# Optimization experiments

Hardware: AMD Instinct MI355X
Metric: run time of the kernel (lower is better)

Reference implementation:

```python
import jax, jax.numpy as jnp
import numpy as np
import math

B, N, OBS, H, A = 4096, 64, 64, 64, 8


def setup_inputs() -> dict:
    key = jax.random.key(0)
    kit = iter(jax.random.split(key, 64))

    def W(o, i):
        return jax.random.normal(next(kit), (o, i), jnp.float32) / float(np.sqrt(i))

    def bvec(o):
        return jax.random.normal(next(kit), (o,), jnp.float32) * 0.01

    inp = {
        "x": jax.random.normal(next(kit), (B, N, OBS), jnp.float32),
        "rnd_nums": jax.random.uniform(next(kit), (B, N), dtype=jnp.float32),
        "idx": jax.random.randint(next(kit), (B, N), 0, N),
    }
    inp.update(embed_w=W(H, OBS), embed_b=bvec(H))
    for pre in ("ia", "c1", "c2"):  # init_attn, consensus_attn1, consensus_attn2 (1 head)
        inp.update({pre + "_wq": W(H, H), pre + "_bq": bvec(H),
                    pre + "_wk": W(H, H), pre + "_bk": bvec(H),
                    pre + "_wv": W(H, H), pre + "_bv": bvec(H),
                    pre + "_wo": W(H, H), pre + "_bo": bvec(H)})
    inp.update(msg_w=W(H, H), msg_b=bvec(H), st_w=W(H, H), st_b=bvec(H),
               mean_w=W(A, 2 * H), mean_b=bvec(A), ls_w=W(A, 2 * H), ls_b=bvec(A))
    return inp


def reference(x, rnd_nums, idx, embed_w, embed_b,
              ia_wq, ia_bq, ia_wk, ia_bk, ia_wv, ia_bv, ia_wo, ia_bo,
              msg_w, msg_b, st_w, st_b,
              c1_wq, c1_bq, c1_wk, c1_bk, c1_wv, c1_bv, c1_wo, c1_bo,
              c2_wq, c2_bq, c2_wk, c2_bk, c2_wv, c2_bv, c2_wo, c2_bo,
              mean_w, mean_b, ls_w, ls_b):
    h = embed_w.shape[0]
    scale = 1.0 / math.sqrt(h)
    lrelu = lambda z: jax.nn.leaky_relu(z, 0.2)

    # ---- initial state estimation (self-attention over agents) ----
    e = lrelu(x @ embed_w.T + embed_b)                       # [B,N,H]
    q = e @ ia_wq.T + ia_bq
    k = e @ ia_wk.T + ia_bk
    v = e @ ia_wv.T + ia_bv
    w = jax.nn.softmax(jnp.einsum('bih,bjh->bij', q, k) * scale, axis=-1)
    attn = jnp.tanh(jnp.einsum('bij,bjh->bih', w, v) @ ia_wo.T + ia_bo)
    messages = attn @ msg_w.T + msg_b                        # [B,N,H]
    temp = attn @ st_w.T + st_b                              # [B,N,H]

    # ---- consensus masks: mg[b,i,j] = (r_i > a_i) | (r_j > a_i) ----
    a = jnp.take_along_axis(rnd_nums, idx, axis=1)           # agent_rnd per agent slot [B,N]
    gi = rnd_nums[:, :, None] > a[:, :, None]
    gj = rnd_nums[:, None, :] > a[:, :, None]
    mg = (gi | gj).astype(x.dtype)                           # [B,N,N]
    ml = 1.0 - mg

    def cons(mask, wq, bq, wk, bk, wv, bv, wo, bo):
        # single-token query (agent temp state) attends over zero-masked messages;
        # masked tokens contribute k = bk, v = bv (bias survives the zeroing).
        qq = temp @ wq.T + bq                                # [B,N,H]
        km = messages @ wk.T                                 # [B,N,H] (no bias; folded below)
        vm = messages @ wv.T
        s = (mask * jnp.einsum('bih,bjh->bij', qq, km) + (qq @ bk)[:, :, None]) * scale
        wgt = jax.nn.softmax(s, axis=-1)                     # [B,N_agents,N_tokens]
        ctx = jnp.einsum('bij,bjh->bih', wgt * mask, vm) + bv
        return ctx @ wo.T + bo

    o1 = cons(mg, c1_wq, c1_bq, c1_wk, c1_bk, c1_wv, c1_bv, c1_wo, c1_bo)
    o2 = cons(ml, c2_wq, c2_bq, c2_wk, c2_bk, c2_wv, c2_bv, c2_wo, c2_bo)
    out = lrelu(jnp.concatenate([o1, o2], axis=-1))          # [B,N,2H]
    mean = out @ mean_w.T + mean_b                           # [B,N,A]
    logstd = jnp.clip(out @ ls_w.T + ls_b, -20.0, 2.0)
    return mean, jnp.exp(logstd)
```

## Files before the change

### kernel.cpp

```cpp
#include <hip/hip_runtime.h>

namespace {

typedef __bf16 bf16x8 __attribute__((ext_vector_type(8)));
typedef float f32x4 __attribute__((ext_vector_type(4)));
typedef unsigned int uint4v __attribute__((ext_vector_type(4)));

#define MFMA16(a,b,c) __builtin_amdgcn_mfma_f32_16x16x32_bf16((a),(b),(c),0,0,0)

constexpr float SCALE = 0.125f;

constexpr int WS_HW  = 57344;
constexpr int WS_NV  = 61440;
constexpr int WS_VEC = 63488;
constexpr int WS_SC  = 65536;

__device__ __forceinline__ int PI(int c){ return 4*(c&15) + (c>>4); }
__device__ __forceinline__ int PINV(int p){ return 16*(p&3) + (p>>2); }

__device__ __forceinline__ unsigned short f2b(float f){
  return __builtin_bit_cast(unsigned short, (__bf16)f);
}
__device__ __forceinline__ unsigned pack2(float a, float b){
  return (unsigned)f2b(a) | ((unsigned)f2b(b)<<16);
}
template<int ACT>
__device__ __forceinline__ float actf(float v){
  if constexpr (ACT==1) return v>0.f ? v : 0.2f*v;
  else if constexpr (ACT==2) return 1.f - 2.f/(__expf(2.f*v)+1.f);
  else return v;
}

struct PrepP {
  const float *embed_w, *mean_w, *ls_w;
  const float *ia_wq, *ia_bq, *ia_wk, *ia_wv, *ia_wo, *ia_bv, *ia_bo;
  const float *c1_wq, *c1_bq, *c1_wk, *c1_bk, *c1_wv, *c1_bv, *c1_wo, *c1_bo;
  const float *c2_wq, *c2_bq, *c2_wk, *c2_bk, *c2_wv, *c2_bv, *c2_wo, *c2_bo;
  const float *msg_w, *msg_b, *st_w, *st_b;
  char* ws;
};

__device__ void mmAB_f32(const float* A, const float* B, float* O){
  const int t=threadIdx.x, r=t>>2, c0=(t&3)*16;
  float acc[16];
  #pragma unroll
  for(int j=0;j<16;j++) acc[j]=0.f;
  for(int h=0;h<64;h++){
    const float a=A[r*64+h];
    #pragma unroll
    for(int j=0;j<16;j++) acc[j]=fmaf(a,B[h*64+c0+j],acc[j]);
  }
  #pragma unroll
  for(int j=0;j<16;j++) O[r*64+c0+j]=acc[j];
}
__device__ void mmAB_bf(const float* A, const float* B, __bf16* D){
  const int t=threadIdx.x, r=t>>2, c0=(t&3)*16;
  float acc[16];
  #pragma unroll
  for(int j=0;j<16;j++) acc[j]=0.f;
  for(int h=0;h<64;h++){
    const float a=A[r*64+h];
    #pragma unroll
    for(int j=0;j<16;j++) acc[j]=fmaf(a,B[h*64+c0+j],acc[j]);
  }
  #pragma unroll
  for(int j=0;j<16;j++) D[r*64+PI(c0+j)]=(__bf16)acc[j];
}
__device__ void mmTA_bfx(const float* A, const float* B, __bf16* D){
  const int t=threadIdx.x, a=t>>2, b0=(t&3)*16;
  float acc[16];
  #pragma unroll
  for(int j=0;j<16;j++) acc[j]=0.f;
  for(int h=0;h<64;h++){
    const float av=A[h*64+a];
    #pragma unroll
    for(int j=0;j<16;j++) acc[j]=fmaf(av,B[h*64+b0+j],acc[j]);
  }
  #pragma unroll
  for(int j=0;j<16;j++) D[a*64 + (PI(b0+j) ^ ((a&7)<<3))]=(__bf16)acc[j];
}

__global__ void prep_kernel(PrepP q){
  __shared__ float PF[2][4096];
  __shared__ float hv[64], gv[64];
  const int job=blockIdx.x, t=threadIdx.x;
  char* ws=q.ws;
  float* VECF=(float*)(ws+WS_VEC);
  float* SCF =(float*)(ws+WS_SC);
  __bf16* NVD=(__bf16*)(ws+WS_NV);

  if(job==0){
    __bf16* emb=(__bf16*)(ws+0*8192);
    #pragma unroll
    for(int i=0;i<16;i++){
      const int idx=t*16+i, o=idx>>6, pp=idx&63;
      emb[idx]=(__bf16)q.embed_w[o*64 + PINV(pp ^ ((o&7)<<3))];
    }
    __bf16* hw=(__bf16*)(ws+WS_HW);
    #pragma unroll
    for(int i=0;i<8;i++){
      const int flat=t*8+i, o=flat>>7, qq=flat&127, half=qq>>6, pp=qq&63;
      const float v=(o<8)?q.mean_w[o*128+half*64+PINV(pp)]
                         :q.ls_w[(o-8)*128+half*64+PINV(pp)];
      hw[flat]=(__bf16)v;
    }
    #pragma unroll
    for(int i=0;i<3;i++){ const int id=t*3+i; if(id<768) NVD[256+id]=(__bf16)0.f; }
  } else if(job==1){
    mmTA_bfx(q.ia_wk, q.ia_wq, (__bf16*)(ws+1*8192));
    if(t<64){ float s=0; for(int h=0;h<64;h++) s+=q.ia_wk[h*64+t]*q.ia_bq[h]; VECF[t]=s; }
  } else if(job==2){
    mmAB_bf(q.ia_wo, q.ia_wv, (__bf16*)(ws+2*8192));
    if(t<64){ float s=q.ia_bo[t]; for(int h=0;h<64;h++) s+=q.ia_wo[t*64+h]*q.ia_bv[h];
              VECF[64+t]=s; }
  } else if(job==3 || job==5){
    const int cons=(job==3)?0:1;
    const float *wq=cons?q.c2_wq:q.c1_wq, *bq=cons?q.c2_bq:q.c1_bq;
    const float *wk=cons?q.c2_wk:q.c1_wk, *bk=cons?q.c2_bk:q.c1_bk;
    mmAB_f32(wq, q.st_w, PF[0]);
    if(t<64){ float s=bq[t]; for(int k=0;k<64;k++) s+=wq[t*64+k]*q.st_b[k]; hv[t]=s; }
    __syncthreads();
    mmAB_f32(wk, q.msg_w, PF[1]);
    if(t<64){ float s=0; for(int k=0;k<64;k++) s+=wk[t*64+k]*q.msg_b[k]; gv[t]=s; }
    __syncthreads();
    mmTA_bfx(PF[1], PF[0], (__bf16*)(ws+(cons?5:3)*8192));
    if(t<64){
      float s=0; for(int h=0;h<64;h++) s+=PF[1][h*64+t]*hv[h];
      VECF[128+cons*64+t]=s;
      float s0=0,s1=0;
      for(int h=0;h<64;h++){ s0+=PF[0][h*64+t]*gv[h]; s1+=PF[0][h*64+t]*bk[h]; }
      NVD[(2*cons  )*64+PI(t)]=(__bf16)s0;
      NVD[(2*cons+1)*64+PI(t)]=(__bf16)s1;
    }
    if(t==0){
      float c=0,hb=0;
      for(int i=0;i<64;i++){ c+=hv[i]*gv[i]; hb+=hv[i]*bk[i]; }
      SCF[2*cons]=c; SCF[2*cons+1]=hb;
    }
  } else {
    const int cons=(job==4)?0:1;
    const float *wo=cons?q.c2_wo:q.c1_wo, *wvv=cons?q.c2_wv:q.c1_wv;
    const float *bv=cons?q.c2_bv:q.c1_bv, *bo=cons?q.c2_bo:q.c1_bo;
    mmAB_f32(wo, wvv, PF[0]);
    if(t<64){ float s=bo[t]; for(int h=0;h<64;h++) s+=wo[t*64+h]*bv[h];
              VECF[320+cons*128+t]=s; }
    __syncthreads();
    mmAB_bf(PF[0], q.msg_w, (__bf16*)(ws+(cons?6:4)*8192));
    if(t<64){ float s=0; for(int k=0;k<64;k++) s+=PF[0][t*64+k]*q.msg_b[k];
              VECF[256+cons*128+t]=s; }
  }
}

struct Params {
  const float *x, *rnd; const int *idx;
  const float *embed_b, *mean_b, *ls_b;
  const char* ws; float* out; int std_off;
};

__device__ __forceinline__ bf16x8 fragld(const char* buf, int row, int kb){
  const int byte = row*128 + (kb ^ ((row&7)<<4));
  return __builtin_bit_cast(bf16x8, *reinterpret_cast<const uint4v*>(buf + byte));
}
__device__ __forceinline__ bf16x8 gld(const char* a){
  return __builtin_bit_cast(bf16x8, *reinterpret_cast<const uint4v*>(a));
}
__device__ __forceinline__ void stageT(const char* src, char* L, int t){
  __builtin_amdgcn_global_load_lds(
      (const __attribute__((address_space(1))) unsigned int*)(src + t*16),
      (__attribute__((address_space(3))) unsigned int*)(L + (t>>6)*1024), 16, 0, 0);
}
__device__ __forceinline__ void loadB_lds(const char* Bl, bf16x8* bf, int fr, int fg){
  #pragma unroll
  for(int n=0;n<4;n++){
    bf[2*n]   = fragld(Bl, n*16+fr, fg*16);
    bf[2*n+1] = fragld(Bl, n*16+fr, 64+fg*16);
  }
}

__device__ __forceinline__ void mm_AB(const char* A, const char* Bl, f32x4* acc,
                                      int fr,int fg,int wv4){
  const bf16x8 a0=fragld(A,16*wv4+fr,fg*16), a1=fragld(A,16*wv4+fr,64+fg*16);
  #pragma unroll
  for(int n=0;n<4;n++){
    acc[n]=MFMA16(a0, fragld(Bl,n*16+fr,fg*16),    acc[n]);
    acc[n]=MFMA16(a1, fragld(Bl,n*16+fr,64+fg*16), acc[n]);
  }
}
__device__ __forceinline__ void mm_rAB(bf16x8 a0, bf16x8 a1, const bf16x8* bf,
                                       f32x4* acc){
  #pragma unroll
  for(int n=0;n<4;n++){
    acc[n]=MFMA16(a0, bf[2*n],   acc[n]);
    acc[n]=MFMA16(a1, bf[2*n+1], acc[n]);
  }
}

template<int ACT>
__device__ __forceinline__ void store_cb(char* C, const f32x4* acc, const float* bz,
                                         int fr,int fg,int wv4){
  #pragma unroll
  for(int r=0;r<4;r++){
    const int R=16*wv4+4*fg+r;
    float v[4];
    #pragma unroll
    for(int n=0;n<4;n++) v[n]=actf<ACT>(acc[n][r]+bz[n]);
    uint2 pk; pk.x=pack2(v[0],v[1]); pk.y=pack2(v[2],v[3]);
    *reinterpret_cast<uint2*>(C + R*128 + ((8*fr)^((R&7)<<4))) = pk;
  }
}
__device__ __forceinline__ void store_rb(char* C, const f32x4* acc, const float* dR,
                                         int fr,int fg,int wv4){
  #pragma unroll
  for(int r=0;r<4;r++){
    const int R=16*wv4+4*fg+r;
    float v[4];
    #pragma unroll
    for(int n=0;n<4;n++) v[n]=acc[n][r]+dR[r];
    uint2 pk; pk.x=pack2(v[0],v[1]); pk.y=pack2(v[2],v[3]);
    *reinterpret_cast<uint2*>(C + R*128 + ((8*fr)^((R&7)<<4))) = pk;
  }
}

template<int MODE>
__device__ __forceinline__ void ssoft(const char* Aq, const bf16x8* bf, char* P,
                                      const float* rs, const float* as_,
                                      const float* zu, const float* zq,
                                      float cu, float cq,
                                      int fr,int fg,int wv4){
  f32x4 acc[4];
  #pragma unroll
  for(int n=0;n<4;n++) acc[n]=f32x4{0.f,0.f,0.f,0.f};
  const bf16x8 a0=fragld(Aq,16*wv4+fr,fg*16), a1=fragld(Aq,16*wv4+fr,64+fg*16);
  #pragma unroll
  for(int n=0;n<4;n++){
    acc[n]=MFMA16(a0, bf[2*n],   acc[n]);
    acc[n]=MFMA16(a1, bf[2*n+1], acc[n]);
  }
  unsigned mbits=0;
  if constexpr(MODE!=0){
    float rc[4], aR[4], ucR[4], qtR[4]; bool giR[4];
    #pragma unroll
    for(int n=0;n<4;n++) rc[n]=rs[n*16+fr];
    #pragma unroll
    for(int r=0;r<4;r++){
      const int R=16*wv4+4*fg+r;
      aR[r]=as_[R]; giR[r]=rs[R]>aR[r];
      ucR[r]=zu[R]+cu; qtR[r]=zq[R]+cq;
    }
    #pragma unroll
    for(int n=0;n<4;n++){
      #pragma unroll
      for(int r=0;r<4;r++){
        bool mv=giR[r]||(rc[n]>aR[r]);
        if constexpr(MODE==2) mv=!mv;
        const float mf=mv?1.f:0.f;
        if(mv) mbits|=1u<<(n*4+r);
        acc[n][r]=(mf*(acc[n][r]+ucR[r])+qtR[r])*SCALE;
      }
    }
  }
  float sm[4]={0,0,0,0};
  #pragma unroll
  for(int n=0;n<4;n++){
    #pragma unroll
    for(int r=0;r<4;r++){
      float e;
      if constexpr(MODE==0) e=__expf(acc[n][r]*SCALE);
      else e=__expf(acc[n][r]);
      acc[n][r]=e; sm[r]+=e;
    }
  }
  #pragma unroll
  for(int m=1;m<16;m<<=1){
    #pragma unroll
    for(int r=0;r<4;r++) sm[r]+=__shfl_xor(sm[r],m);
  }
  #pragma unroll
  for(int r=0;r<4;r++){
    const int R=16*wv4+4*fg+r;
    const float ri=1.f/sm[r];
    float v[4];
    #pragma unroll
    for(int n=0;n<4;n++){
      float e=acc[n][r]*ri;
      if constexpr(MODE!=0) e=(mbits&(1u<<(n*4+r)))?e:0.f;
      v[n]=e;
    }
    uint2 pk; pk.x=pack2(v[0],v[1]); pk.y=pack2(v[2],v[3]);
    *reinterpret_cast<uint2*>(P + R*128 + ((8*fr)^((R&7)<<4))) = pk;
  }
}

__global__ __launch_bounds__(512,4) void rap_kernel(Params p, int Bb){
  __shared__ __align__(16) char Bact[2][3][8192];
  __shared__ __align__(16) char WSst[2][8192];
  __shared__ float rnd_s[2][64], a_s[2][64], zbuf[2][4][64];
  const int t=threadIdx.x;
  const int fr=t&15, fg=(t>>4)&3, wv=t>>6, l=t&63;
  const int item=wv>>2, wv4=wv&3;
  const int b0=blockIdx.x*2;
  const int bi=(b0+item<Bb)?(b0+item):(Bb-1);
  const char* ws=p.ws;
  const float* VECF=(const float*)(ws+WS_VEC);
  const float* SCF =(const float*)(ws+WS_SC);
  char* A0=Bact[item][0]; char* A1=Bact[item][1]; char* A2=Bact[item][2];
  char* WO1=WSst[item];
  bf16x8 bfv[8];

  stageT(ws+0*8192, WSst[0], t);
  stageT(ws+1*8192, WSst[1], t);
  if(t<128){
    const int it2=t>>6, i2=t&63;
    const int bb=(b0+it2<Bb)?(b0+it2):(Bb-1);
    rnd_s[it2][i2]=p.rnd[bb*64+i2];
    a_s[it2][i2]  =p.rnd[bb*64+p.idx[bb*64+i2]];
  }
  {
    const float* Gx=p.x+(size_t)bi*4096;
    #pragma unroll
    for(int j=0;j<2;j++){
      const int lf=j*64+l, R=16*wv4+(lf>>3), k=lf&7;
      const float2 L0=*reinterpret_cast<const float2*>(Gx+R*64+2*k);
      const float2 L1=*reinterpret_cast<const float2*>(Gx+R*64+16+2*k);
      const float2 L2=*reinterpret_cast<const float2*>(Gx+R*64+32+2*k);
      const float2 L3=*reinterpret_cast<const float2*>(Gx+R*64+48+2*k);
      uint4 pk;
      pk.x=pack2(L0.x,L1.x); pk.y=pack2(L2.x,L3.x);
      pk.z=pack2(L0.y,L1.y); pk.w=pack2(L2.y,L3.y);
      *reinterpret_cast<uint4*>(A0 + R*128 + ((16*k)^((R&7)<<4)))=pk;
    }
  }
  __syncthreads();
  { f32x4 acc[4]={{0,0,0,0},{0,0,0,0},{0,0,0,0},{0,0,0,0}};
    mm_AB(A0, WSst[0], acc, fr,fg,wv4);
    float bz[4];
    #pragma unroll
    for(int n=0;n<4;n++) bz[n]=p.embed_b[n*16+fr];
    store_cb<1>(A1, acc, bz, fr,fg,wv4); }
  { f32x4 acc[4]={{0,0,0,0},{0,0,0,0},{0,0,0,0},{0,0,0,0}};
    mm_AB(A1, WSst[1], acc, fr,fg,wv4);
    float bz[4];
    #pragma unroll
    for(int n=0;n<4;n++) bz[n]=VECF[n*16+fr];
    store_cb<0>(A0, acc, bz, fr,fg,wv4); }
  __syncthreads();
  stageT(ws+3*8192, WSst[0], t);
  stageT(ws+5*8192, WSst[1], t);
  const bf16x8 aVo0=gld(ws+2*8192+(16*wv4+fr)*128+fg*16);
  const bf16x8 aVo1=gld(ws+2*8192+(16*wv4+fr)*128+64+fg*16);
  loadB_lds(A1, bfv, fr, fg);
  ssoft<0>(A0, bfv, A0, nullptr,nullptr,nullptr,nullptr,0.f,0.f, fr,fg,wv4);
  { f32x4 acc[4]={{0,0,0,0},{0,0,0,0},{0,0,0,0},{0,0,0,0}};
    mm_rAB(aVo0, aVo1, bfv, acc);
    const float bz[4]={0,0,0,0};
    store_cb<0>(A2, acc, bz, fr,fg,wv4); }
  __syncthreads();
  const bf16x8 nv0=gld(ws+WS_NV+fr*128+fg*16);
  const bf16x8 nv1=gld(ws+WS_NV+fr*128+64+fg*16);
  { f32x4 acc[4]={{0,0,0,0},{0,0,0,0},{0,0,0,0},{0,0,0,0}};
    mm_AB(A0, A2, acc, fr,fg,wv4);
    float bz[4];
    #pragma unroll
    for(int n=0;n<4;n++) bz[n]=VECF[64+n*16+fr];
    store_cb<2>(A1, acc, bz, fr,fg,wv4); }
  { const bf16x8 a0=fragld(A1,16*wv4+fr,fg*16), a1=fragld(A1,16*wv4+fr,64+fg*16);
    f32x4 acc[4]={{0,0,0,0},{0,0,0,0},{0,0,0,0},{0,0,0,0}};
    #pragma unroll
    for(int n=0;n<4;n++){
      acc[n]=MFMA16(a0, fragld(WSst[0],n*16+fr,fg*16),    acc[n]);
      acc[n]=MFMA16(a1, fragld(WSst[0],n*16+fr,64+fg*16), acc[n]);
    }
    f32x4 za={0,0,0,0};
    za=MFMA16(a0, nv0, za);
    za=MFMA16(a1, nv1, za);
    if(fr<4){
      #pragma unroll
      for(int r=0;r<4;r++) zbuf[item][fr][16*wv4+4*fg+r]=za[r];
    }
    float bz[4];
    #pragma unroll
    for(int n=0;n<4;n++) bz[n]=VECF[128+n*16+fr];
    store_cb<0>(A0, acc, bz, fr,fg,wv4); }
  __syncthreads();
  const bf16x8 aN10=gld(ws+4*8192+(16*wv4+fr)*128+fg*16);
  const bf16x8 aN11=gld(ws+4*8192+(16*wv4+fr)*128+64+fg*16);
  loadB_lds(A1, bfv, fr, fg);
  ssoft<1>(A0, bfv, A0, rnd_s[item], a_s[item], zbuf[item][0], zbuf[item][1],
           SCF[0], SCF[1], fr,fg,wv4);
  { f32x4 acc[4]={{0,0,0,0},{0,0,0,0},{0,0,0,0},{0,0,0,0}};
    mm_rAB(aN10, aN11, bfv, acc);
    float dR[4];
    #pragma unroll
    for(int r=0;r<4;r++) dR[r]=VECF[256+16*wv4+4*fg+r];
    store_rb(A2, acc, dR, fr,fg,wv4); }
  __syncthreads();
  f32x4 o1acc[4]={{0,0,0,0},{0,0,0,0},{0,0,0,0},{0,0,0,0}};
  mm_AB(A0, A2, o1acc, fr,fg,wv4);
  { f32x4 acc[4]={{0,0,0,0},{0,0,0,0},{0,0,0,0},{0,0,0,0}};
    const bf16x8 a0=fragld(A1,16*wv4+fr,fg*16), a1=fragld(A1,16*wv4+fr,64+fg*16);
    #pragma unroll
    for(int n=0;n<4;n++){
      acc[n]=MFMA16(a0, fragld(WSst[1],n*16+fr,fg*16),    acc[n]);
      acc[n]=MFMA16(a1, fragld(WSst[1],n*16+fr,64+fg*16), acc[n]);
    }
    float bz[4];
    #pragma unroll
    for(int n=0;n<4;n++) bz[n]=VECF[192+n*16+fr];
    store_cb<0>(A0, acc, bz, fr,fg,wv4); }
  __syncthreads();
  { float bz[4];
    #pragma unroll
    for(int n=0;n<4;n++) bz[n]=VECF[320+n*16+fr];
    store_cb<1>(WO1, o1acc, bz, fr,fg,wv4); }
  const bf16x8 aN20=gld(ws+6*8192+(16*wv4+fr)*128+fg*16);
  const bf16x8 aN21=gld(ws+6*8192+(16*wv4+fr)*128+64+fg*16);
  loadB_lds(A1, bfv, fr, fg);
  ssoft<2>(A0, bfv, A0, rnd_s[item], a_s[item], zbuf[item][2], zbuf[item][3],
           SCF[2], SCF[3], fr,fg,wv4);
  { f32x4 acc[4]={{0,0,0,0},{0,0,0,0},{0,0,0,0},{0,0,0,0}};
    mm_rAB(aN20, aN21, bfv, acc);
    float dR[4];
    #pragma unroll
    for(int r=0;r<4;r++) dR[r]=VECF[384+16*wv4+4*fg+r];
    store_rb(A2, acc, dR, fr,fg,wv4); }
  __syncthreads();
  bf16x8 hw[4];
  #pragma unroll
  for(int kt=0;kt<4;kt++) hw[kt]=gld(ws+WS_HW + fr*256 + kt*64 + fg*16);
  { f32x4 acc[4]={{0,0,0,0},{0,0,0,0},{0,0,0,0},{0,0,0,0}};
    mm_AB(A0, A2, acc, fr,fg,wv4);
    float bz[4];
    #pragma unroll
    for(int n=0;n<4;n++) bz[n]=VECF[448+n*16+fr];
    store_cb<1>(A1, acc, bz, fr,fg,wv4); }
  { f32x4 acc={0,0,0,0};
    #pragma unroll
    for(int kt=0;kt<4;kt++){
      const bf16x8 af=fragld(kt<2?WO1:A1, 16*wv4+fr, (kt&1)*64+fg*16);
      acc=MFMA16(af, hw[kt], acc);
    }
    if(b0+item<Bb){
      const float bz=(fr<8)?p.mean_b[fr]:p.ls_b[fr-8];
      #pragma unroll
      for(int r=0;r<4;r++){
        const int R=16*wv4+4*fg+r;
        const int g=((b0+item)*64+R)*8;
        float v=acc[r]+bz;
        if(fr<8) p.out[g+fr]=v;
        else{ v=fminf(fmaxf(v,-20.f),2.f); p.out[p.std_off+g+(fr-8)]=__expf(v); }
      }
    }
  }
}

}

extern "C" void kernel_launch(void* const* d_in, const int* in_sizes, int n_in,
                              void* d_out, int out_size, void* d_ws, size_t ws_size,
                              hipStream_t stream){
  (void)n_in; (void)out_size; (void)ws_size;
  PrepP q;
  q.embed_w=(const float*)d_in[3];
  q.ia_wq=(const float*)d_in[5];  q.ia_bq=(const float*)d_in[6];
  q.ia_wk=(const float*)d_in[7];
  q.ia_wv=(const float*)d_in[9];  q.ia_bv=(const float*)d_in[10];
  q.ia_wo=(const float*)d_in[11]; q.ia_bo=(const float*)d_in[12];
  q.c1_wq=(const float*)d_in[13]; q.c1_bq=(const float*)d_in[14];
  q.c1_wk=(const float*)d_in[15]; q.c1_bk=(const float*)d_in[16];
  q.c1_wv=(const float*)d_in[17]; q.c1_bv=(const float*)d_in[18];
  q.c1_wo=(const float*)d_in[19]; q.c1_bo=(const float*)d_in[20];
  q.c2_wq=(const float*)d_in[21]; q.c2_bq=(const float*)d_in[22];
  q.c2_wk=(const float*)d_in[23]; q.c2_bk=(const float*)d_in[24];
  q.c2_wv=(const float*)d_in[25]; q.c2_bv=(const float*)d_in[26];
  q.c2_wo=(const float*)d_in[27]; q.c2_bo=(const float*)d_in[28];
  q.msg_w=(const float*)d_in[29]; q.msg_b=(const float*)d_in[30];
  q.st_w =(const float*)d_in[31]; q.st_b =(const float*)d_in[32];
  q.mean_w=(const float*)d_in[33]; q.ls_w=(const float*)d_in[35];
  q.ws=(char*)d_ws;
  prep_kernel<<<dim3(7), dim3(256), 0, stream>>>(q);

  Params p;
  p.x  =(const float*)d_in[0];
  p.rnd=(const float*)d_in[1];
  p.idx=(const int*)  d_in[2];
  p.embed_b=(const float*)d_in[4];
  p.mean_b =(const float*)d_in[34];
  p.ls_b   =(const float*)d_in[36];
  p.ws=(const char*)d_ws;
  p.out=(float*)d_out;
  const int Bb=in_sizes[0]/4096;
  p.std_off=Bb*64*8;
  const int nb=(Bb+1)/2;
  rap_kernel<<<dim3(nb), dim3(512), 0, stream>>>(p, Bb);
}
```

Baseline: 115.8 us.

## Relax block barriers to LDS-only waits and interleave score/value matmuls

Replaces __syncthreads with inline-asm barriers. Most of them wait only on lgkmcnt, so outstanding global loads into registers can stay in flight across the barrier. Each attention stage is split into the score MFMA and a softmax post-pass, and the value/message matmul and its store now run between them to overlap MFMA work with the softmax math. It also drops a redundant reload of the shared B fragments from LDS in the second consensus stage, since that LDS tile has not changed. The risk is correctness if any barrier actually depended on pending global memory operations, and register pressure rises because the score accumulators stay live longer.

Result: slower. 121.7 us (+5.1%).

```diff
diff --git a/kernel.cpp b/kernel.cpp
--- a/kernel.cpp
+++ b/kernel.cpp
@@ -29,6 +29,13 @@
   if constexpr (ACT==1) return v>0.f ? v : 0.2f*v;
   else if constexpr (ACT==2) return 1.f - 2.f/(__expf(2.f*v)+1.f);
   else return v;
+}
+
+__device__ __forceinline__ void bar_lgkm(){
+  asm volatile("s_waitcnt lgkmcnt(0)\n\ts_barrier" ::: "memory");
+}
+__device__ __forceinline__ void bar_full(){
+  asm volatile("s_waitcnt vmcnt(0) lgkmcnt(0)\n\ts_barrier" ::: "memory");
 }
 
 struct PrepP {
@@ -186,14 +193,23 @@
     acc[n]=MFMA16(a1, fragld(Bl,n*16+fr,64+fg*16), acc[n]);
   }
 }
-__device__ __forceinline__ void mm_rAB(bf16x8 a0, bf16x8 a1, const bf16x8* bf,
-                                       f32x4* acc){
+__device__ __forceinline__ void mm_ABr(const char* A, const bf16x8* bf, f32x4* acc,
+                                       int fr,int fg,int wv4){
+  const bf16x8 a0=fragld(A,16*wv4+fr,fg*16), a1=fragld(A,16*wv4+fr,64+fg*16);
   #pragma unroll
   for(int n=0;n<4;n++){
     acc[n]=MFMA16(a0, bf[2*n],   acc[n]);
     acc[n]=MFMA16(a1, bf[2*n+1], acc[n]);
   }
 }
+__device__ __forceinline__ void mm_rAB(bf16x8 a0, bf16x8 a1, const bf16x8* bf,
+                                       f32x4* acc){
+  #pragma unroll
+  for(int n=0;n<4;n++){
+    acc[n]=MFMA16(a0, bf[2*n],   acc[n]);
+    acc[n]=MFMA16(a1, bf[2*n+1], acc[n]);
+  }
+}
 
 template<int ACT>
 __device__ __forceinline__ void store_cb(char* C, const f32x4* acc, const float* bz,
@@ -221,21 +237,21 @@
   }
 }
 
-template<int MODE>
-__device__ __forceinline__ void ssoft(const char* Aq, const bf16x8* bf, char* P,
-                                      const float* rs, const float* as_,
-                                      const float* zu, const float* zq,
-                                      float cu, float cq,
-                                      int fr,int fg,int wv4){
-  f32x4 acc[4];
-  #pragma unroll
-  for(int n=0;n<4;n++) acc[n]=f32x4{0.f,0.f,0.f,0.f};
+__device__ __forceinline__ void score_mm(const char* Aq, const bf16x8* bf, f32x4* acc,
+                                         int fr,int fg,int wv4){
   const bf16x8 a0=fragld(Aq,16*wv4+fr,fg*16), a1=fragld(Aq,16*wv4+fr,64+fg*16);
   #pragma unroll
   for(int n=0;n<4;n++){
     acc[n]=MFMA16(a0, bf[2*n],   acc[n]);
     acc[n]=MFMA16(a1, bf[2*n+1], acc[n]);
   }
+}
+template<int MODE>
+__device__ __forceinline__ void soft_post(f32x4* acc, char* P,
+                                          const float* rs, const float* as_,
+                                          const float* zu, const float* zq,
+                                          float cu, float cq,
+                                          int fr,int fg,int wv4){
   unsigned mbits=0;
   if constexpr(MODE!=0){
     float rc[4], aR[4], ucR[4], qtR[4]; bool giR[4];
@@ -330,7 +346,7 @@
       *reinterpret_cast<uint4*>(A0 + R*128 + ((16*k)^((R&7)<<4)))=pk;
     }
   }
-  __syncthreads();
+  bar_full();
   { f32x4 acc[4]={{0,0,0,0},{0,0,0,0},{0,0,0,0},{0,0,0,0}};
     mm_AB(A0, WSst[0], acc, fr,fg,wv4);
     float bz[4];
@@ -343,18 +359,20 @@
     #pragma unroll
     for(int n=0;n<4;n++) bz[n]=VECF[n*16+fr];
     store_cb<0>(A0, acc, bz, fr,fg,wv4); }
-  __syncthreads();
+  bar_lgkm();
   stageT(ws+3*8192, WSst[0], t);
   stageT(ws+5*8192, WSst[1], t);
   const bf16x8 aVo0=gld(ws+2*8192+(16*wv4+fr)*128+fg*16);
   const bf16x8 aVo1=gld(ws+2*8192+(16*wv4+fr)*128+64+fg*16);
   loadB_lds(A1, bfv, fr, fg);
-  ssoft<0>(A0, bfv, A0, nullptr,nullptr,nullptr,nullptr,0.f,0.f, fr,fg,wv4);
-  { f32x4 acc[4]={{0,0,0,0},{0,0,0,0},{0,0,0,0},{0,0,0,0}};
-    mm_rAB(aVo0, aVo1, bfv, acc);
-    const float bz[4]={0,0,0,0};
-    store_cb<0>(A2, acc, bz, fr,fg,wv4); }
-  __syncthreads();
+  { f32x4 sacc[4]={{0,0,0,0},{0,0,0,0},{0,0,0,0},{0,0,0,0}};
+    score_mm(A0, bfv, sacc, fr,fg,wv4);
+    { f32x4 acc[4]={{0,0,0,0},{0,0,0,0},{0,0,0,0},{0,0,0,0}};
+      mm_rAB(aVo0, aVo1, bfv, acc);
+      const float bz[4]={0,0,0,0};
+      store_cb<0>(A2, acc, bz, fr,fg,wv4); }
+    soft_post<0>(sacc, A0, nullptr,nullptr,nullptr,nullptr,0.f,0.f, fr,fg,wv4); }
+  bar_full();
   const bf16x8 nv0=gld(ws+WS_NV+fr*128+fg*16);
   const bf16x8 nv1=gld(ws+WS_NV+fr*128+64+fg*16);
   { f32x4 acc[4]={{0,0,0,0},{0,0,0,0},{0,0,0,0},{0,0,0,0}};
@@ -381,19 +399,21 @@
     #pragma unroll
     for(int n=0;n<4;n++) bz[n]=VECF[128+n*16+fr];
     store_cb<0>(A0, acc, bz, fr,fg,wv4); }
-  __syncthreads();
+  bar_lgkm();
   const bf16x8 aN10=gld(ws+4*8192+(16*wv4+fr)*128+fg*16);
   const bf16x8 aN11=gld(ws+4*8192+(16*wv4+fr)*128+64+fg*16);
   loadB_lds(A1, bfv, fr, fg);
-  ssoft<1>(A0, bfv, A0, rnd_s[item], a_s[item], zbuf[item][0], zbuf[item][1],
-           SCF[0], SCF[1], fr,fg,wv4);
-  { f32x4 acc[4]={{0,0,0,0},{0,0,0,0},{0,0,0,0},{0,0,0,0}};
-    mm_rAB(aN10, aN11, bfv, acc);
-    float dR[4];
-    #pragma unroll
-    for(int r=0;r<4;r++) dR[r]=VECF[256+16*wv4+4*fg+r];
-    store_rb(A2, acc, dR, fr,fg,wv4); }
-  __syncthreads();
+  { f32x4 sacc[4]={{0,0,0,0},{0,0,0,0},{0,0,0,0},{0,0,0,0}};
+    score_mm(A0, bfv, sacc, fr,fg,wv4);
+    { f32x4 acc[4]={{0,0,0,0},{0,0,0,0},{0,0,0,0},{0,0,0,0}};
+      mm_rAB(aN10, aN11, bfv, acc);
+      float dR[4];
+      #pragma unroll
+      for(int r=0;r<4;r++) dR[r]=VECF[256+16*wv4+4*fg+r];
+      store_rb(A2, acc, dR, fr,fg,wv4); }
+    soft_post<1>(sacc, A0, rnd_s[item], a_s[item], zbuf[item][0], zbuf[item][1],
+                 SCF[0], SCF[1], fr,fg,wv4); }
+  bar_lgkm();
   f32x4 o1acc[4]={{0,0,0,0},{0,0,0,0},{0,0,0,0},{0,0,0,0}};
   mm_AB(A0, A2, o1acc, fr,fg,wv4);
   { f32x4 acc[4]={{0,0,0,0},{0,0,0,0},{0,0,0,0},{0,0,0,0}};
@@ -407,23 +427,24 @@
     #pragma unroll
     for(int n=0;n<4;n++) bz[n]=VECF[192+n*16+fr];
     store_cb<0>(A0, acc, bz, fr,fg,wv4); }
-  __syncthreads();
+  bar_lgkm();
   { float bz[4];
     #pragma unroll
     for(int n=0;n<4;n++) bz[n]=VECF[320+n*16+fr];
     store_cb<1>(WO1, o1acc, bz, fr,fg,wv4); }
   const bf16x8 aN20=gld(ws+6*8192+(16*wv4+fr)*128+fg*16);
   const bf16x8 aN21=gld(ws+6*8192+(16*wv4+fr)*128+64+fg*16);
-  loadB_lds(A1, bfv, fr, fg);
-  ssoft<2>(A0, bfv, A0, rnd_s[item], a_s[item], zbuf[item][2], zbuf[item][3],
-           SCF[2], SCF[3], fr,fg,wv4);
-  { f32x4 acc[4]={{0,0,0,0},{0,0,0,0},{0,0,0,0},{0,0,0,0}};
-    mm_rAB(aN20, aN21, bfv, acc);
-    float dR[4];
-    #pragma unroll
-    for(int r=0;r<4;r++) dR[r]=VECF[384+16*wv4+4*fg+r];
-    store_rb(A2, acc, dR, fr,fg,wv4); }
-  __syncthreads();
+  { f32x4 sacc[4]={{0,0,0,0},{0,0,0,0},{0,0,0,0},{0,0,0,0}};
+    score_mm(A0, bfv, sacc, fr,fg,wv4);
+    { f32x4 acc[4]={{0,0,0,0},{0,0,0,0},{0,0,0,0},{0,0,0,0}};
+      mm_rAB(aN20, aN21, bfv, acc);
+      float dR[4];
+      #pragma unroll
+      for(int r=0;r<4;r++) dR[r]=VECF[384+16*wv4+4*fg+r];
+      store_rb(A2, acc, dR, fr,fg,wv4); }
+    soft_post<2>(sacc, A0, rnd_s[item], a_s[item], zbuf[item][2], zbuf[item][3],
+                 SCF[2], SCF[3], fr,fg,wv4); }
+  bar_lgkm();
   bf16x8 hw[4];
   #pragma unroll
   for(int kt=0;kt<4;kt++) hw[kt]=gld(ws+WS_HW + fr*256 + kt*64 + fg*16);
```
